# Optimization experiments

Hardware: AMD Instinct MI355X
Metric: run time of the kernel (lower is better)

Reference implementation:

```python
import jax, jax.numpy as jnp
import numpy as np

N, L, S, H, E, D = 4, 1024, 1024, 16, 64, 64
NUM_POS = 2  # adjacency matrix: 0 = not adjacent, 1 = adjacent


def setup_inputs() -> dict:
    key = jax.random.key(0)
    kq, kk, kv, kt, kp = jax.random.split(key, 5)
    return {
        "queries": jax.random.normal(kq, (N, L, H, E), dtype=jnp.float32),
        "keys": jax.random.normal(kk, (N, S, H, E), dtype=jnp.float32),
        "values": jax.random.normal(kv, (N, S, H, D), dtype=jnp.float32),
        "attn_mask": jnp.zeros((L, S), dtype=jnp.float32),          # additive attention mask
        "key_len_mask": jnp.zeros((N, S), dtype=jnp.float32),       # additive key-length mask
        "pos_table": jax.random.normal(kt, (NUM_POS, H), dtype=jnp.float32),  # per-head graph pos bias
        "pos": jax.random.randint(kp, (N, L, S), 0, NUM_POS),        # adjacency matrix
    }


def reference(queries, keys, values, attn_mask, key_len_mask, pos_table, pos):
    E_dim = queries.shape[-1]
    softmax_temp = 1.0 / jnp.sqrt(jnp.asarray(E_dim, dtype=queries.dtype))
    # scores: [N, H, L, S]
    QK = jnp.einsum("nlhe,nshe->nhls", queries, keys)
    QK = QK + attn_mask[None, None, :, :]
    QK = QK + key_len_mask[:, None, None, :]
    QK = softmax_temp * QK
    # graph positional encoding: per-head bias looked up from adjacency matrix
    # pos_table[pos] -> [N, L, S, H] -> [N, H, L, S]
    QK = QK + jnp.transpose(pos_table[pos], (0, 3, 1, 2))
    A = jax.nn.softmax(QK, axis=-1)  # dropout is identity in eval/reference
    V = jnp.einsum("nhls,nshd->nlhd", A, values)
    return V
```

## Files before the change

kernel.cpp:

```cpp
#include <hip/hip_runtime.h>


typedef __attribute__((ext_vector_type(8))) __bf16 bf16x8;
typedef __attribute__((ext_vector_type(16))) float f32x16;
typedef __attribute__((ext_vector_type(4))) unsigned int u32x4;

#define TEMP2 (0.125f * 1.4426950408889634f)
#define LG2E 1.4426950408889634f

static __device__ __forceinline__ unsigned short f2bf(float x) {
  unsigned int u = __builtin_bit_cast(unsigned int, x);
  u += 0x7FFFu + ((u >> 16) & 1u);
  return (unsigned short)(u >> 16);
}
static __device__ __forceinline__ unsigned int cvtpk(float lo, float hi) {
  unsigned int r;
  asm("v_cvt_pk_bf16_f32 %0, %1, %2" : "=v"(r) : "v"(lo), "v"(hi));
  return r;
}
static __device__ __forceinline__ void gload16(const void* g, void* l) {
  __builtin_amdgcn_global_load_lds((const __attribute__((address_space(1))) void*)g,
                                   (__attribute__((address_space(3))) void*)l, 16, 0, 0);
}
static __device__ __forceinline__ void plswap(unsigned int& a, unsigned int& b) {
  asm("v_permlane32_swap_b32 %0, %1" : "+v"(a), "+v"(b));
}

__global__ __launch_bounds__(256) void k_prep(
    const int* __restrict__ pos, unsigned int* __restrict__ pospk,
    const float* __restrict__ K, unsigned short* __restrict__ Kp,
    const float* __restrict__ V, unsigned short* __restrict__ Vt,
    const float* __restrict__ mask, const float* __restrict__ klm,
    int* __restrict__ cmflag) {
  __shared__ float ld[64][65];
  int b = blockIdx.x;
  int tid = threadIdx.x;
  if (b < 256) {
    int idx = b * 256 + tid;
    int s = (idx >> 4) & 1023;
    const float* src = K + idx * 64;
    unsigned short row[64];
#pragma unroll
    for (int j = 0; j < 16; ++j) {
      float4 v = *(const float4*)(src + j * 4);
      row[j*4+0] = f2bf(v.x); row[j*4+1] = f2bf(v.y);
      row[j*4+2] = f2bf(v.z); row[j*4+3] = f2bf(v.w);
    }
    int n = idx >> 14, h = idx & 15;
    unsigned short* dst = Kp + ((n * 16 + h) * 1024 + s) * 64;
#pragma unroll
    for (int bb = 0; bb < 8; ++bb) {
      int pb = bb ^ (s & 7);
      *(u32x4*)(dst + pb * 8) = *(const u32x4*)(&row[bb * 8]);
    }
  } else if (b < 1280) {
    int vb = b - 256;
    int t = vb & 15, h = (vb >> 4) & 15, n = vb >> 8;
    {
      int s = tid >> 2, dq = (tid & 3) * 16;
      const float* src = V + ((n * 1024 + t * 64 + s) * 16 + h) * 64 + dq;
#pragma unroll
      for (int j = 0; j < 4; ++j) {
        float4 v = *(const float4*)(src + j * 4);
        ld[s][dq + j*4 + 0] = v.x; ld[s][dq + j*4 + 1] = v.y;
        ld[s][dq + j*4 + 2] = v.z; ld[s][dq + j*4 + 3] = v.w;
      }
    }
    __syncthreads();
    {
      int d = tid >> 2, sq = (tid & 3) * 16;
      unsigned short vals[16];
#pragma unroll
      for (int k = 0; k < 16; ++k) vals[k] = f2bf(ld[sq + k][d]);
      unsigned short* dst = Vt + ((n * 16 + h) * 64 + d) * 1024 + t * 64;
#pragma unroll
      for (int cb = 0; cb < 2; ++cb) {
        int blk = (sq >> 3) + cb;
        int pb = blk ^ (d & 7);
        *(u32x4*)(dst + pb * 8) = *(const u32x4*)(&vals[cb * 8]);
      }
    }
  } else if (b < 1536) {
    if (!cmflag) return;
    int base = ((b - 1280) * 256 + tid) * 16;
    const float* m = mask + base;
    float acc = 0.f;
#pragma unroll
    for (int j = 0; j < 4; ++j) {
      float4 v = *(const float4*)(m + j * 4);
      acc += __builtin_fabsf(v.x) + __builtin_fabsf(v.y) +
             __builtin_fabsf(v.z) + __builtin_fabsf(v.w);
    }
    unsigned long long bal = __ballot(acc != 0.f);
    if ((tid & 63) == 0 && bal != 0ull) atomicOr(cmflag, 1);
  } else if (b == 1536) {
    if (!cmflag) return;
    const float* m = klm + tid * 16;
    float acc = 0.f;
#pragma unroll
    for (int j = 0; j < 4; ++j) {
      float4 v = *(const float4*)(m + j * 4);
      acc += __builtin_fabsf(v.x) + __builtin_fabsf(v.y) +
             __builtin_fabsf(v.z) + __builtin_fabsf(v.w);
    }
    unsigned long long bal = __ballot(acc != 0.f);
    if ((tid & 63) == 0 && bal != 0ull) atomicOr(cmflag, 1);
  } else {
    int gi = (b - 1537) * 256 + tid;
    int v = pos[gi];
    unsigned long long m = __ballot(v & 1);
    int lane = tid & 63;
    if (lane == 0 || lane == 32) {
      int n = gi >> 20, l = (gi >> 10) & 1023, sw = (gi & 1023) >> 5;
      pospk[(n * 32 + sw) * 1024 + l] =
          (lane == 0) ? (unsigned int)m : (unsigned int)(m >> 32);
    }
  }
}

__global__ __launch_bounds__(512) void k_attn(
    const float* __restrict__ Q, const float* __restrict__ mask,
    const float* __restrict__ klm, const float* __restrict__ ptab,
    const unsigned int* __restrict__ pospk,
    const unsigned short* __restrict__ Kp, const unsigned short* __restrict__ Vt,
    const int* __restrict__ cmf,
    float* __restrict__ out) {
  __shared__ __align__(16) unsigned short KBA[2][4096];
  __shared__ __align__(16) unsigned short KBB[2][4096];
  __shared__ __align__(16) unsigned short VBA[2][4096];
  __shared__ __align__(16) unsigned short VBB[2][4096];
  __shared__ __align__(16) unsigned short VBC[2][4096];

  int bid = blockIdx.x;
  int nh = bid & 63;
  int n = nh >> 4, h = nh & 15, lblk = bid >> 6;
  int tid = threadIdx.x;
  int w8 = tid >> 6, lane = tid & 63;
  int g = w8 >> 2, w4 = w8 & 3;
  int l31 = lane & 31, h5 = lane >> 5;
  int l = lblk * 128 + w4 * 32 + l31;
  const int hcm = cmf ? *cmf : 1;

  const float* qrow = Q + ((n * 1024 + l) * 16 + h) * 64;
  bf16x8 qf[4];
#pragma unroll
  for (int ke = 0; ke < 4; ++ke) {
    float4 a = *(const float4*)(qrow + ke * 16 + h5 * 8);
    float4 bq = *(const float4*)(qrow + ke * 16 + h5 * 8 + 4);
    u32x4 pk;
    pk[0] = cvtpk(a.x * TEMP2, a.y * TEMP2);
    pk[1] = cvtpk(a.z * TEMP2, a.w * TEMP2);
    pk[2] = cvtpk(bq.x * TEMP2, bq.y * TEMP2);
    pk[3] = cvtpk(bq.z * TEMP2, bq.w * TEMP2);
    qf[ke] = __builtin_bit_cast(bf16x8, pk);
  }
  const float delta2 = (ptab[16 + h] - ptab[h]) * LG2E;

  float mrun = -1e30f, lrun = 0.f;
  f32x16 Oc0 = {0,0,0,0,0,0,0,0,0,0,0,0,0,0,0,0};
  f32x16 Oc1 = {0,0,0,0,0,0,0,0,0,0,0,0,0,0,0,0};
  u32x4 pfA = {0,0,0,0}, pfB = {0,0,0,0}, pfC = {0,0,0,0}, pfD = {0,0,0,0};

  const unsigned short* KpB = Kp + nh * 65536;
  const unsigned short* VtB = Vt + nh * 65536;
  const float* mrowB = mask + l * 1024 + g * 512;
  const float* krowB = klm + n * 1024 + g * 512;
  const unsigned int* posB = pospk + (n * 32 + g * 16) * 1024 + l;
  const int h4 = h5 * 4;

  const int x7 = l31 & 7;
  const int co0 = ((0 + h5) ^ x7) * 8;
  const int co1 = ((2 + h5) ^ x7) * 8;
  const int co2 = ((4 + h5) ^ x7) * 8;
  const int co3 = ((6 + h5) ^ x7) * 8;
  const int rb = l31 * 64;

  const unsigned short* kS = KpB + g * 32768 + w4 * 1024 + lane * 8;
  const unsigned short* vS = VtB + (w4 * 16 + (lane >> 3)) * 1024 + g * 512 + (lane & 7) * 8;
  const int kD = w4 * 1024 + lane * 8;

#define BF(x) __builtin_bit_cast(bf16x8, x)
#define MFMA(A, B, C) __builtin_amdgcn_mfma_f32_32x32x16_bf16(A, B, C, 0, 0, 0)
#define LDB(ARR, OFF) BF(*(const u32x4*)&ARR[g][(OFF)])

#pragma unroll
  for (int j = 0; j < 2; ++j) {
    gload16(kS + j * 512, &KBA[g][kD + j * 512]);
    gload16(vS + j * 8192, &VBA[g][kD + j * 512]);
  }
  __syncthreads();

#define BODY(T, KR, KW, VR, VW, DO_PV, STG)                                    \
  {                                                                            \
    unsigned pwx = posB[((T) * 2) * 1024];                  \
    unsigned pwy = posB[((T) * 2 + 1) * 1024];                                 \
          \
    if (STG) {                                                                 \
      _Pragma("unroll")                                                        \
      for (int j = 0; j < 2; ++j) {                                            \
        gload16(kS + ((T) + 1) * 4096 + j * 512, &KW[g][kD + j * 512]);        \
        gload16(vS + ((T) + 1) * 64 + j * 8192, &VW[g][kD + j * 512]);         \
      }                                                                        \
    }                                                                          \
                     \
    f32x16 sv0 = {0,0,0,0,0,0,0,0,0,0,0,0,0,0,0,0};                            \
    f32x16 sv1 = {0,0,0,0,0,0,0,0,0,0,0,0,0,0,0,0};                            \
    __builtin_amdgcn_s_setprio(1);                                             \
    sv0 = MFMA(LDB(KR, rb + co0), qf[0], sv0);                                 \
    sv1 = MFMA(LDB(KR, rb + 2048 + co0), qf[0], sv1);                          \
    if (DO_PV) {                                                               \
      Oc0 = MFMA(LDB(VR, rb + co0), BF(pfA), Oc0);                             \
      Oc1 = MFMA(LDB(VR, rb + 2048 + co0), BF(pfA), Oc1);                      \
    }                                                                          \
    sv0 = MFMA(LDB(KR, rb + co1), qf[1], sv0);                                 \
    sv1 = MFMA(LDB(KR, rb + 2048 + co1), qf[1], sv1);                          \
    if (DO_PV) {                                                               \
      Oc0 = MFMA(LDB(VR, rb + co1), BF(pfB), Oc0);                             \
      Oc1 = MFMA(LDB(VR, rb + 2048 + co1), BF(pfB), Oc1);                      \
    }                                                                          \
    sv0 = MFMA(LDB(KR, rb + co2), qf[2], sv0);                                 \
    sv1 = MFMA(LDB(KR, rb + 2048 + co2), qf[2], sv1);                          \
    if (DO_PV) {                                                               \
      Oc0 = MFMA(LDB(VR, rb + co2), BF(pfC), Oc0);                             \
      Oc1 = MFMA(LDB(VR, rb + 2048 + co2), BF(pfC), Oc1);                      \
    }                                                                          \
    sv0 = MFMA(LDB(KR, rb + co3), qf[3], sv0);                                 \
    sv1 = MFMA(LDB(KR, rb + 2048 + co3), qf[3], sv1);                          \
    if (DO_PV) {                                                               \
      Oc0 = MFMA(LDB(VR, rb + co3), BF(pfD), Oc0);                             \
      Oc1 = MFMA(LDB(VR, rb + 2048 + co3), BF(pfD), Oc1);                      \
    }                                                                          \
    __builtin_amdgcn_s_setprio(0);                                             \
               \
    if (hcm) {                                                                 \
      _Pragma("unroll")                                                        \
      for (int r2 = 0; r2 < 4; ++r2) {                                         \
        float4 mv0 = *(const float4*)(mrowB + (T) * 64 + r2 * 8 + h4);         \
        float4 kv0 = *(const float4*)(krowB + (T) * 64 + r2 * 8 + h4);         \
        float4 mv1 = *(const float4*)(mrowB + (T) * 64 + 32 + r2 * 8 + h4);    \
        float4 kv1 = *(const float4*)(krowB + (T) * 64 + 32 + r2 * 8 + h4);    \
        sv0[r2 * 4 + 0] += (mv0.x + kv0.x) * TEMP2;                            \
        sv0[r2 * 4 + 1] += (mv0.y + kv0.y) * TEMP2;                            \
        sv0[r2 * 4 + 2] += (mv0.z + kv0.z) * TEMP2;                            \
        sv0[r2 * 4 + 3] += (mv0.w + kv0.w) * TEMP2;                            \
        sv1[r2 * 4 + 0] += (mv1.x + kv1.x) * TEMP2;                            \
        sv1[r2 * 4 + 1] += (mv1.y + kv1.y) * TEMP2;                            \
        sv1[r2 * 4 + 2] += (mv1.z + kv1.z) * TEMP2;                            \
        sv1[r2 * 4 + 3] += (mv1.w + kv1.w) * TEMP2;                            \
      }                                                                        \
    }                                                                          \
    {                                                                          \
      unsigned pws0 = pwx >> h4;                                               \
      unsigned pws1 = pwy >> h4;                                               \
      _Pragma("unroll")                                                        \
      for (int r2 = 0; r2 < 4; ++r2)                                           \
        _Pragma("unroll")                                                      \
        for (int i = 0; i < 4; ++i) {                                          \
          float bit0 = (float)((pws0 >> (r2 * 8 + i)) & 1u);                   \
          float bit1 = (float)((pws1 >> (r2 * 8 + i)) & 1u);                   \
          sv0[r2 * 4 + i] = fmaf(bit0, delta2, sv0[r2 * 4 + i]);               \
          sv1[r2 * 4 + i] = fmaf(bit1, delta2, sv1[r2 * 4 + i]);               \
        }                                                                      \
    }                                                                          \
                      \
    {                                                                          \
      float m8[8];                                                             \
      _Pragma("unroll")                                                        \
      for (int i = 0; i < 8; ++i)                                              \
        m8[i] = fmaxf(fmaxf(sv0[2 * i], sv0[2 * i + 1]),                       \
                      fmaxf(sv1[2 * i], sv1[2 * i + 1]));                      \
      float m4a = fmaxf(m8[0], m8[1]), m4b = fmaxf(m8[2], m8[3]);              \
      float m4c = fmaxf(m8[4], m8[5]), m4d = fmaxf(m8[6], m8[7]);              \
      float tmax = fmaxf(fmaxf(m4a, m4b), fmaxf(m4c, m4d));                    \
      tmax = fmaxf(tmax, __shfl_xor(tmax, 32));                                \
      if (!__all(tmax <= mrun + 4.0f)) {                                       \
        float mnew = fmaxf(mrun, tmax);                                        \
        float sc = __builtin_amdgcn_exp2f(mrun - mnew);                        \
        lrun *= sc;                                                            \
        Oc0 *= sc; Oc1 *= sc;                                                  \
        mrun = mnew;                                                           \
      }                                                                        \
      float s8[8];                                                             \
      _Pragma("unroll")                                                        \
      for (int i = 0; i < 8; ++i) {                                            \
        float p0 = __builtin_amdgcn_exp2f(sv0[2 * i] - mrun);                  \
        float p1 = __builtin_amdgcn_exp2f(sv0[2 * i + 1] - mrun);              \
        float p2 = __builtin_amdgcn_exp2f(sv1[2 * i] - mrun);                  \
        float p3 = __builtin_amdgcn_exp2f(sv1[2 * i + 1] - mrun);              \
        sv0[2 * i] = p0; sv0[2 * i + 1] = p1;                                  \
        sv1[2 * i] = p2; sv1[2 * i + 1] = p3;                                  \
        s8[i] = (p0 + p1) + (p2 + p3);                                         \
      }                                                                        \
      float s4a = s8[0] + s8[1], s4b = s8[2] + s8[3];                          \
      float s4c = s8[4] + s8[5], s4d = s8[6] + s8[7];                          \
      lrun += (s4a + s4b) + (s4c + s4d);    \
    }                                                                          \
                    \
    {                                                                          \
      unsigned a0 = cvtpk(sv0[0], sv0[1]),   a1 = cvtpk(sv0[2], sv0[3]);       \
      unsigned a2 = cvtpk(sv0[4], sv0[5]),   a3 = cvtpk(sv0[6], sv0[7]);       \
      plswap(a0, a2); plswap(a1, a3);                                          \
      pfA[0] = a0; pfA[1] = a1; pfA[2] = a2; pfA[3] = a3;                      \
      unsigned b0_ = cvtpk(sv0[8], sv0[9]),   b1_ = cvtpk(sv0[10], sv0[11]);   \
      unsigned b2_ = cvtpk(sv0[12], sv0[13]), b3_ = cvtpk(sv0[14], sv0[15]);   \
      plswap(b0_, b2_); plswap(b1_, b3_);                                      \
      pfB[0] = b0_; pfB[1] = b1_; pfB[2] = b2_; pfB[3] = b3_;                  \
      unsigned c0 = cvtpk(sv1[0], sv1[1]),   c1 = cvtpk(sv1[2], sv1[3]);       \
      unsigned c2 = cvtpk(sv1[4], sv1[5]),   c3 = cvtpk(sv1[6], sv1[7]);       \
      plswap(c0, c2); plswap(c1, c3);                                          \
      pfC[0] = c0; pfC[1] = c1; pfC[2] = c2; pfC[3] = c3;                      \
      unsigned d0 = cvtpk(sv1[8], sv1[9]),   d1 = cvtpk(sv1[10], sv1[11]);     \
      unsigned d2 = cvtpk(sv1[12], sv1[13]), d3 = cvtpk(sv1[14], sv1[15]);     \
      plswap(d0, d2); plswap(d1, d3);                                          \
      pfD[0] = d0; pfD[1] = d1; pfD[2] = d2; pfD[3] = d3;                      \
    }                                                                          \
    if (STG) __syncthreads();        \
  }

  BODY( 0, KBA, KBB, VBA, VBB, 0, 1)
  BODY( 1, KBB, KBA, VBA, VBC, 1, 1)
  BODY( 2, KBA, KBB, VBB, VBA, 1, 1)
  BODY( 3, KBB, KBA, VBC, VBB, 1, 1)
  BODY( 4, KBA, KBB, VBA, VBC, 1, 1)
  BODY( 5, KBB, KBA, VBB, VBA, 1, 1)
  BODY( 6, KBA, KBB, VBC, VBB, 1, 1)
  BODY( 7, KBB, KBB, VBA, VBB, 1, 0)
#undef BODY

  __builtin_amdgcn_s_setprio(1);
  Oc0 = MFMA(LDB(VBB, rb + co0), BF(pfA), Oc0);
  Oc1 = MFMA(LDB(VBB, rb + 2048 + co0), BF(pfA), Oc1);
  Oc0 = MFMA(LDB(VBB, rb + co1), BF(pfB), Oc0);
  Oc1 = MFMA(LDB(VBB, rb + 2048 + co1), BF(pfB), Oc1);
  Oc0 = MFMA(LDB(VBB, rb + co2), BF(pfC), Oc0);
  Oc1 = MFMA(LDB(VBB, rb + 2048 + co2), BF(pfC), Oc1);
  Oc0 = MFMA(LDB(VBB, rb + co3), BF(pfD), Oc0);
  Oc1 = MFMA(LDB(VBB, rb + 2048 + co3), BF(pfD), Oc1);
  __builtin_amdgcn_s_setprio(0);
#undef MFMA
#undef BF
#undef LDB

  float lw = lrun + __shfl_xor(lrun, 32);
  __syncthreads();
#pragma unroll
  for (int r = 0; r < 2; ++r) {
    if (g == 1 && (w4 >> 1) == r) {
      float* row = ((w4 & 1) ? (float*)VBB : (float*)VBA) + lane * 36;
#pragma unroll
      for (int r2 = 0; r2 < 4; ++r2) {
        *(float4*)(row + r2 * 4) =
            make_float4(Oc0[4*r2+0], Oc0[4*r2+1], Oc0[4*r2+2], Oc0[4*r2+3]);
        *(float4*)(row + 16 + r2 * 4) =
            make_float4(Oc1[4*r2+0], Oc1[4*r2+1], Oc1[4*r2+2], Oc1[4*r2+3]);
      }
      row[32] = mrun;
      row[33] = lw;
    }
    __syncthreads();
    if (g == 0 && (w4 >> 1) == r) {
      const float* row = ((w4 & 1) ? (float*)VBB : (float*)VBA) + lane * 36;
      float m1 = row[32], l1 = row[33];
      float mm = fmaxf(mrun, m1);
      float s0e = __builtin_amdgcn_exp2f(mrun - mm);
      float s1e = __builtin_amdgcn_exp2f(m1 - mm);
      float ltot = lw * s0e + l1 * s1e;
      float inv = 1.0f / ltot;
      float* orow = out + ((n * 1024 + l) * 16 + h) * 64;
#pragma unroll
      for (int r2 = 0; r2 < 4; ++r2) {
        float4 o;
        o.x = (Oc0[4*r2+0] * s0e + row[r2*4+0] * s1e) * inv;
        o.y = (Oc0[4*r2+1] * s0e + row[r2*4+1] * s1e) * inv;
        o.z = (Oc0[4*r2+2] * s0e + row[r2*4+2] * s1e) * inv;
        o.w = (Oc0[4*r2+3] * s0e + row[r2*4+3] * s1e) * inv;
        *(float4*)(orow + r2 * 8 + h4) = o;
        o.x = (Oc1[4*r2+0] * s0e + row[16+r2*4+0] * s1e) * inv;
        o.y = (Oc1[4*r2+1] * s0e + row[16+r2*4+1] * s1e) * inv;
        o.z = (Oc1[4*r2+2] * s0e + row[16+r2*4+2] * s1e) * inv;
        o.w = (Oc1[4*r2+3] * s0e + row[16+r2*4+3] * s1e) * inv;
        *(float4*)(orow + 32 + r2 * 8 + h4) = o;
      }
    }
    __syncthreads();
  }
}

extern "C" void kernel_launch(void* const* d_in, const int* in_sizes, int n_in,
                              void* d_out, int out_size, void* d_ws, size_t ws_size,
                              hipStream_t stream) {
  const float* Q    = (const float*)d_in[0];
  const float* K    = (const float*)d_in[1];
  const float* V    = (const float*)d_in[2];
  const float* mask = (const float*)d_in[3];
  const float* klm  = (const float*)d_in[4];
  const float* ptab = (const float*)d_in[5];
  const int*   pos  = (const int*)d_in[6];
  float* out = (float*)d_out;

  char* ws = (char*)d_ws;
  unsigned int*   pospk = (unsigned int*)ws;
  unsigned short* Kp    = (unsigned short*)(ws + (1 << 19));
  unsigned short* Vt    = (unsigned short*)(ws + (1 << 19) + (8 << 20));
  int*            cmf   = (int*)(ws + (1 << 19) + (16 << 20));
  const size_t need_flag = (size_t)(1 << 19) + (size_t)(16 << 20) + 64;
  const bool use_flag = ws_size >= need_flag;
  if (!use_flag) cmf = nullptr;

  if (use_flag) hipMemsetAsync(cmf, 0, 4, stream);
  k_prep<<<17921, 256, 0, stream>>>(pos, pospk, K, Kp, V, Vt, mask, klm, cmf);
  k_attn<<<512, 512, 0, stream>>>(Q, mask, klm, ptab, pospk, Kp, Vt, cmf, out);
}
```

Baseline: 64.38 us.

## Fuse prep and attention into one cooperative kernel with grid sync

Replaces the memset, the prep kernel and the attention kernel with a single cooperative launch. In the first phase each block converts K to bf16, transposes V through LDS, packs adjacency bits and checks whether any mask is nonzero. A grid-wide sync then lets the same blocks run the attention body, which is turned into a shared macro. The aim is to remove two extra launches and the inter-kernel gap. The cost is a grid barrier, and the fused kernel needs at least two resident blocks per CU; if that check or the cooperative launch fails, it falls back to the old path.

```diff
diff --git a/kernel.cpp b/kernel.cpp
--- a/kernel.cpp
+++ b/kernel.cpp
@@ -1,5 +1,8 @@
 #include <hip/hip_runtime.h>
-
+#include <hip/hip_cooperative_groups.h>
+
+
+namespace cg = cooperative_groups;
 
 typedef __attribute__((ext_vector_type(8))) __bf16 bf16x8;
 typedef __attribute__((ext_vector_type(16))) float f32x16;
@@ -118,83 +121,124 @@
   }
 }
 
-__global__ __launch_bounds__(512) void k_attn(
-    const float* __restrict__ Q, const float* __restrict__ mask,
-    const float* __restrict__ klm, const float* __restrict__ ptab,
-    const unsigned int* __restrict__ pospk,
-    const unsigned short* __restrict__ Kp, const unsigned short* __restrict__ Vt,
-    const int* __restrict__ cmf,
-    float* __restrict__ out) {
-  __shared__ __align__(16) unsigned short KBA[2][4096];
-  __shared__ __align__(16) unsigned short KBB[2][4096];
-  __shared__ __align__(16) unsigned short VBA[2][4096];
-  __shared__ __align__(16) unsigned short VBB[2][4096];
-  __shared__ __align__(16) unsigned short VBC[2][4096];
-
-  int bid = blockIdx.x;
-  int nh = bid & 63;
-  int n = nh >> 4, h = nh & 15, lblk = bid >> 6;
-  int tid = threadIdx.x;
-  int w8 = tid >> 6, lane = tid & 63;
-  int g = w8 >> 2, w4 = w8 & 3;
-  int l31 = lane & 31, h5 = lane >> 5;
-  int l = lblk * 128 + w4 * 32 + l31;
-  const int hcm = cmf ? *cmf : 1;
-
-  const float* qrow = Q + ((n * 1024 + l) * 16 + h) * 64;
-  bf16x8 qf[4];
-#pragma unroll
-  for (int ke = 0; ke < 4; ++ke) {
-    float4 a = *(const float4*)(qrow + ke * 16 + h5 * 8);
-    float4 bq = *(const float4*)(qrow + ke * 16 + h5 * 8 + 4);
-    u32x4 pk;
-    pk[0] = cvtpk(a.x * TEMP2, a.y * TEMP2);
-    pk[1] = cvtpk(a.z * TEMP2, a.w * TEMP2);
-    pk[2] = cvtpk(bq.x * TEMP2, bq.y * TEMP2);
-    pk[3] = cvtpk(bq.z * TEMP2, bq.w * TEMP2);
-    qf[ke] = __builtin_bit_cast(bf16x8, pk);
-  }
-  const float delta2 = (ptab[16 + h] - ptab[h]) * LG2E;
-
-  float mrun = -1e30f, lrun = 0.f;
-  f32x16 Oc0 = {0,0,0,0,0,0,0,0,0,0,0,0,0,0,0,0};
-  f32x16 Oc1 = {0,0,0,0,0,0,0,0,0,0,0,0,0,0,0,0};
-  u32x4 pfA = {0,0,0,0}, pfB = {0,0,0,0}, pfC = {0,0,0,0}, pfD = {0,0,0,0};
-
-  const unsigned short* KpB = Kp + nh * 65536;
-  const unsigned short* VtB = Vt + nh * 65536;
-  const float* mrowB = mask + l * 1024 + g * 512;
-  const float* krowB = klm + n * 1024 + g * 512;
-  const unsigned int* posB = pospk + (n * 32 + g * 16) * 1024 + l;
-  const int h4 = h5 * 4;
-
-  const int x7 = l31 & 7;
-  const int co0 = ((0 + h5) ^ x7) * 8;
-  const int co1 = ((2 + h5) ^ x7) * 8;
-  const int co2 = ((4 + h5) ^ x7) * 8;
-  const int co3 = ((6 + h5) ^ x7) * 8;
-  const int rb = l31 * 64;
-
-  const unsigned short* kS = KpB + g * 32768 + w4 * 1024 + lane * 8;
-  const unsigned short* vS = VtB + (w4 * 16 + (lane >> 3)) * 1024 + g * 512 + (lane & 7) * 8;
-  const int kD = w4 * 1024 + lane * 8;
+#define ATTN_MAIN(HCMEXPR)                                                     \
+  int nh = bid & 63;                                                           \
+  int n = nh >> 4, h = nh & 15, lblk = bid >> 6;                               \
+  int w8 = tid >> 6, lane = tid & 63;                                          \
+  int g = w8 >> 2, w4 = w8 & 3;                                                \
+  int l31 = lane & 31, h5 = lane >> 5;                                         \
+  int l = lblk * 128 + w4 * 32 + l31;                                          \
+  const int hcm = (HCMEXPR);                                                   \
+  const float* qrow = Q + ((n * 1024 + l) * 16 + h) * 64;                      \
+  bf16x8 qf[4];                                                                \
+  _Pragma("unroll")                                                            \
+  for (int ke = 0; ke < 4; ++ke) {                                             \
+    float4 a = *(const float4*)(qrow + ke * 16 + h5 * 8);                      \
+    float4 bq = *(const float4*)(qrow + ke * 16 + h5 * 8 + 4);                 \
+    u32x4 pk;                                                                  \
+    pk[0] = cvtpk(a.x * TEMP2, a.y * TEMP2);                                   \
+    pk[1] = cvtpk(a.z * TEMP2, a.w * TEMP2);                                   \
+    pk[2] = cvtpk(bq.x * TEMP2, bq.y * TEMP2);                                 \
+    pk[3] = cvtpk(bq.z * TEMP2, bq.w * TEMP2);                                 \
+    qf[ke] = __builtin_bit_cast(bf16x8, pk);                                   \
+  }                                                                            \
+  const float delta2 = (ptab[16 + h] - ptab[h]) * LG2E;                        \
+  float mrun = -1e30f, lrun = 0.f;                                             \
+  f32x16 Oc0 = {0,0,0,0,0,0,0,0,0,0,0,0,0,0,0,0};                              \
+  f32x16 Oc1 = {0,0,0,0,0,0,0,0,0,0,0,0,0,0,0,0};                              \
+  u32x4 pfA = {0,0,0,0}, pfB = {0,0,0,0}, pfC = {0,0,0,0}, pfD = {0,0,0,0};    \
+  const unsigned short* KpB = Kp + nh * 65536;                                 \
+  const unsigned short* VtB = Vt + nh * 65536;                                 \
+  const float* mrowB = mask + l * 1024 + g * 512;                              \
+  const float* krowB = klm + n * 1024 + g * 512;                               \
+  const unsigned int* posB = pospk + (n * 32 + g * 16) * 1024 + l;             \
+  const int h4 = h5 * 4;                                                       \
+  const int x7 = l31 & 7;                                                      \
+  const int co0 = ((0 + h5) ^ x7) * 8;                                         \
+  const int co1 = ((2 + h5) ^ x7) * 8;                                         \
+  const int co2 = ((4 + h5) ^ x7) * 8;                                         \
+  const int co3 = ((6 + h5) ^ x7) * 8;                                         \
+  const int rb = l31 * 64;                                                     \
+  const unsigned short* kS = KpB + g * 32768 + w4 * 1024 + lane * 8;           \
+  const unsigned short* vS = VtB + (w4 * 16 + (lane >> 3)) * 1024 + g * 512 +  \
+                             (lane & 7) * 8;                                   \
+  const int kD = w4 * 1024 + lane * 8;                                         \
+  _Pragma("unroll")                                                            \
+  for (int j = 0; j < 2; ++j) {                                                \
+    gload16(kS + j * 512, &KBA[g][kD + j * 512]);                              \
+    gload16(vS + j * 8192, &VBA[g][kD + j * 512]);                             \
+  }                                                                            \
+  __syncthreads();                                                             \
+  BODY( 0, KBA, KBB, VBA, VBB, 0, 1)                                           \
+  BODY( 1, KBB, KBA, VBA, VBC, 1, 1)                                           \
+  BODY( 2, KBA, KBB, VBB, VBA, 1, 1)                                           \
+  BODY( 3, KBB, KBA, VBC, VBB, 1, 1)                                           \
+  BODY( 4, KBA, KBB, VBA, VBC, 1, 1)                                           \
+  BODY( 5, KBB, KBA, VBB, VBA, 1, 1)                                           \
+  BODY( 6, KBA, KBB, VBC, VBB, 1, 1)                                           \
+  BODY( 7, KBB, KBB, VBA, VBB, 1, 0)                                           \
+  __builtin_amdgcn_s_setprio(1);                                               \
+  Oc0 = MFMA(LDB(VBB, rb + co0), BF(pfA), Oc0);                                \
+  Oc1 = MFMA(LDB(VBB, rb + 2048 + co0), BF(pfA), Oc1);                         \
+  Oc0 = MFMA(LDB(VBB, rb + co1), BF(pfB), Oc0);                                \
+  Oc1 = MFMA(LDB(VBB, rb + 2048 + co1), BF(pfB), Oc1);                         \
+  Oc0 = MFMA(LDB(VBB, rb + co2), BF(pfC), Oc0);                                \
+  Oc1 = MFMA(LDB(VBB, rb + 2048 + co2), BF(pfC), Oc1);                         \
+  Oc0 = MFMA(LDB(VBB, rb + co3), BF(pfD), Oc0);                                \
+  Oc1 = MFMA(LDB(VBB, rb + 2048 + co3), BF(pfD), Oc1);                         \
+  __builtin_amdgcn_s_setprio(0);                                               \
+  float lw = lrun + __shfl_xor(lrun, 32);                                      \
+  __syncthreads();                                                             \
+  _Pragma("unroll")                                                            \
+  for (int r = 0; r < 2; ++r) {                                                \
+    if (g == 1 && (w4 >> 1) == r) {                                            \
+      float* row = ((w4 & 1) ? (float*)VBB : (float*)VBA) + lane * 36;         \
+      _Pragma("unroll")                                                        \
+      for (int r2 = 0; r2 < 4; ++r2) {                                         \
+        *(float4*)(row + r2 * 4) =                                             \
+            make_float4(Oc0[4*r2+0], Oc0[4*r2+1], Oc0[4*r2+2], Oc0[4*r2+3]);   \
+        *(float4*)(row + 16 + r2 * 4) =                                        \
+            make_float4(Oc1[4*r2+0], Oc1[4*r2+1], Oc1[4*r2+2], Oc1[4*r2+3]);   \
+      }                                                                        \
+      row[32] = mrun;                                                          \
+      row[33] = lw;                                                            \
+    }                                                                          \
+    __syncthreads();                                                           \
+    if (g == 0 && (w4 >> 1) == r) {                                            \
+      const float* row = ((w4 & 1) ? (float*)VBB : (float*)VBA) + lane * 36;   \
+      float m1 = row[32], l1 = row[33];                                        \
+      float mm = fmaxf(mrun, m1);                                              \
+      float s0e = __builtin_amdgcn_exp2f(mrun - mm);                           \
+      float s1e = __builtin_amdgcn_exp2f(m1 - mm);                             \
+      float ltot = lw * s0e + l1 * s1e;                                        \
+      float inv = 1.0f / ltot;                                                 \
+      float* orow = out + ((n * 1024 + l) * 16 + h) * 64;                      \
+      _Pragma("unroll")                                                        \
+      for (int r2 = 0; r2 < 4; ++r2) {                                         \
+        float4 o;                                                              \
+        o.x = (Oc0[4*r2+0] * s0e + row[r2*4+0] * s1e) * inv;                   \
+        o.y = (Oc0[4*r2+1] * s0e + row[r2*4+1] * s1e) * inv;                   \
+        o.z = (Oc0[4*r2+2] * s0e + row[r2*4+2] * s1e) * inv;                   \
+        o.w = (Oc0[4*r2+3] * s0e + row[r2*4+3] * s1e) * inv;                   \
+        *(float4*)(orow + r2 * 8 + h4) = o;                                    \
+        o.x = (Oc1[4*r2+0] * s0e + row[16+r2*4+0] * s1e) * inv;                \
+        o.y = (Oc1[4*r2+1] * s0e + row[16+r2*4+1] * s1e) * inv;                \
+        o.z = (Oc1[4*r2+2] * s0e + row[16+r2*4+2] * s1e) * inv;                \
+        o.w = (Oc1[4*r2+3] * s0e + row[16+r2*4+3] * s1e) * inv;                \
+        *(float4*)(orow + 32 + r2 * 8 + h4) = o;                               \
+      }                                                                        \
+    }                                                                          \
+    __syncthreads();                                                           \
+  }
 
 #define BF(x) __builtin_bit_cast(bf16x8, x)
 #define MFMA(A, B, C) __builtin_amdgcn_mfma_f32_32x32x16_bf16(A, B, C, 0, 0, 0)
 #define LDB(ARR, OFF) BF(*(const u32x4*)&ARR[g][(OFF)])
 
-#pragma unroll
-  for (int j = 0; j < 2; ++j) {
-    gload16(kS + j * 512, &KBA[g][kD + j * 512]);
-    gload16(vS + j * 8192, &VBA[g][kD + j * 512]);
-  }
-  __syncthreads();
-
 #define BODY(T, KR, KW, VR, VW, DO_PV, STG)                                    \
   {                                                                            \
-    unsigned pwx = posB[((T) * 2) * 1024];                  \
+    unsigned pwx = posB[((T) * 2) * 1024];                                     \
     unsigned pwy = posB[((T) * 2 + 1) * 1024];                                 \
-          \
     if (STG) {                                                                 \
       _Pragma("unroll")                                                        \
       for (int j = 0; j < 2; ++j) {                                            \
@@ -202,7 +246,6 @@
         gload16(vS + ((T) + 1) * 64 + j * 8192, &VW[g][kD + j * 512]);         \
       }                                                                        \
     }                                                                          \
-                     \
     f32x16 sv0 = {0,0,0,0,0,0,0,0,0,0,0,0,0,0,0,0};                            \
     f32x16 sv1 = {0,0,0,0,0,0,0,0,0,0,0,0,0,0,0,0};                            \
     __builtin_amdgcn_s_setprio(1);                                             \
@@ -231,7 +274,6 @@
       Oc1 = MFMA(LDB(VR, rb + 2048 + co3), BF(pfD), Oc1);                      \
     }                                                                          \
     __builtin_amdgcn_s_setprio(0);                                             \
-               \
     if (hcm) {                                                                 \
       _Pragma("unroll")                                                        \
       for (int r2 = 0; r2 < 4; ++r2) {                                         \
@@ -262,7 +304,6 @@
           sv1[r2 * 4 + i] = fmaf(bit1, delta2, sv1[r2 * 4 + i]);               \
         }                                                                      \
     }                                                                          \
-                      \
     {                                                                          \
       float m8[8];                                                             \
       _Pragma("unroll")                                                        \
@@ -293,9 +334,8 @@
       }                                                                        \
       float s4a = s8[0] + s8[1], s4b = s8[2] + s8[3];                          \
       float s4c = s8[4] + s8[5], s4d = s8[6] + s8[7];                          \
-      lrun += (s4a + s4b) + (s4c + s4d);    \
-    }                                                                          \
-                    \
+      lrun += (s4a + s4b) + (s4c + s4d);                                       \
+    }                                                                          \
     {                                                                          \
       unsigned a0 = cvtpk(sv0[0], sv0[1]),   a1 = cvtpk(sv0[2], sv0[3]);       \
       unsigned a2 = cvtpk(sv0[4], sv0[5]),   a3 = cvtpk(sv0[6], sv0[7]);       \
@@ -314,76 +354,149 @@
       plswap(d0, d2); plswap(d1, d3);                                          \
       pfD[0] = d0; pfD[1] = d1; pfD[2] = d2; pfD[3] = d3;                      \
     }                                                                          \
-    if (STG) __syncthreads();        \
-  }
-
-  BODY( 0, KBA, KBB, VBA, VBB, 0, 1)
-  BODY( 1, KBB, KBA, VBA, VBC, 1, 1)
-  BODY( 2, KBA, KBB, VBB, VBA, 1, 1)
-  BODY( 3, KBB, KBA, VBC, VBB, 1, 1)
-  BODY( 4, KBA, KBB, VBA, VBC, 1, 1)
-  BODY( 5, KBB, KBA, VBB, VBA, 1, 1)
-  BODY( 6, KBA, KBB, VBC, VBB, 1, 1)
-  BODY( 7, KBB, KBB, VBA, VBB, 1, 0)
-#undef BODY
-
-  __builtin_amdgcn_s_setprio(1);
-  Oc0 = MFMA(LDB(VBB, rb + co0), BF(pfA), Oc0);
-  Oc1 = MFMA(LDB(VBB, rb + 2048 + co0), BF(pfA), Oc1);
-  Oc0 = MFMA(LDB(VBB, rb + co1), BF(pfB), Oc0);
-  Oc1 = MFMA(LDB(VBB, rb + 2048 + co1), BF(pfB), Oc1);
-  Oc0 = MFMA(LDB(VBB, rb + co2), BF(pfC), Oc0);
-  Oc1 = MFMA(LDB(VBB, rb + 2048 + co2), BF(pfC), Oc1);
-  Oc0 = MFMA(LDB(VBB, rb + co3), BF(pfD), Oc0);
-  Oc1 = MFMA(LDB(VBB, rb + 2048 + co3), BF(pfD), Oc1);
-  __builtin_amdgcn_s_setprio(0);
-#undef MFMA
-#undef BF
-#undef LDB
-
-  float lw = lrun + __shfl_xor(lrun, 32);
-  __syncthreads();
-#pragma unroll
-  for (int r = 0; r < 2; ++r) {
-    if (g == 1 && (w4 >> 1) == r) {
-      float* row = ((w4 & 1) ? (float*)VBB : (float*)VBA) + lane * 36;
-#pragma unroll
-      for (int r2 = 0; r2 < 4; ++r2) {
-        *(float4*)(row + r2 * 4) =
-            make_float4(Oc0[4*r2+0], Oc0[4*r2+1], Oc0[4*r2+2], Oc0[4*r2+3]);
-        *(float4*)(row + 16 + r2 * 4) =
-            make_float4(Oc1[4*r2+0], Oc1[4*r2+1], Oc1[4*r2+2], Oc1[4*r2+3]);
+    if (STG) __syncthreads();                                                  \
+  }
+
+__global__ __launch_bounds__(512) void k_attn(
+    const float* __restrict__ Q, const float* __restrict__ mask,
+    const float* __restrict__ klm, const float* __restrict__ ptab,
+    const unsigned int* __restrict__ pospk,
+    const unsigned short* __restrict__ Kp, const unsigned short* __restrict__ Vt,
+    const int* __restrict__ cmf,
+    float* __restrict__ out) {
+  __shared__ __align__(16) unsigned short KBA[2][4096];
+  __shared__ __align__(16) unsigned short KBB[2][4096];
+  __shared__ __align__(16) unsigned short VBA[2][4096];
+  __shared__ __align__(16) unsigned short VBB[2][4096];
+  __shared__ __align__(16) unsigned short VBC[2][4096];
+  int bid = blockIdx.x;
+  int tid = threadIdx.x;
+  ATTN_MAIN(cmf ? *cmf : 1)
+}
+
+__global__ __launch_bounds__(512) void k_fused(
+    const float* __restrict__ Q, const float* __restrict__ K,
+    const float* __restrict__ V, const float* __restrict__ mask,
+    const float* __restrict__ klm, const float* __restrict__ ptab,
+    const int* __restrict__ pos,
+    unsigned int* __restrict__ pospk, unsigned short* __restrict__ Kp,
+    unsigned short* __restrict__ Vt, int* __restrict__ flags,
+    float* __restrict__ out) {
+  __shared__ __align__(16) unsigned short KBA[2][4096];
+  __shared__ __align__(16) unsigned short KBB[2][4096];
+  __shared__ __align__(16) unsigned short VBA[2][4096];
+  __shared__ __align__(16) unsigned short VBB[2][4096];
+  __shared__ __align__(16) unsigned short VBC[2][4096];
+
+  int bid = blockIdx.x;
+  int tid = threadIdx.x;
+  int gt = bid * 512 + tid;
+
+  {
+    int row = gt >> 2, q = gt & 3;
+    int s = (row >> 4) & 1023;
+    const float* src = K + row * 64 + q * 16;
+    unsigned short rv[16];
+#pragma unroll
+    for (int j = 0; j < 4; ++j) {
+      float4 v = *(const float4*)(src + j * 4);
+      rv[j*4+0] = f2bf(v.x); rv[j*4+1] = f2bf(v.y);
+      rv[j*4+2] = f2bf(v.z); rv[j*4+3] = f2bf(v.w);
+    }
+    int n = row >> 14, h = row & 15;
+    unsigned short* dst = Kp + ((n * 16 + h) * 1024 + s) * 64;
+#pragma unroll
+    for (int c = 0; c < 2; ++c) {
+      int bb = q * 2 + c;
+      int pb = bb ^ (s & 7);
+      *(u32x4*)(dst + pb * 8) = *(const u32x4*)(&rv[c * 8]);
+    }
+  }
+  float acc = 0.f;
+  {
+    const float* m = mask + gt * 4;
+    float4 v = *(const float4*)m;
+    acc += __builtin_fabsf(v.x) + __builtin_fabsf(v.y) +
+           __builtin_fabsf(v.z) + __builtin_fabsf(v.w);
+    if (gt < 1024) {
+      float4 kv = *(const float4*)(klm + gt * 4);
+      acc += __builtin_fabsf(kv.x) + __builtin_fabsf(kv.y) +
+             __builtin_fabsf(kv.z) + __builtin_fabsf(kv.w);
+    }
+  }
+  {
+    int r = bid * 8 + (tid >> 6);
+    int n = r >> 10, l = r & 1023;
+    int lane = tid & 63;
+    const int* prow = pos + r * 1024 + lane;
+#pragma unroll
+    for (int j = 0; j < 16; ++j) {
+      unsigned long long m = __ballot(prow[j * 64] & 1);
+      if (lane == 0) pospk[(n * 32 + 2 * j) * 1024 + l] = (unsigned int)m;
+      else if (lane == 32) pospk[(n * 32 + 2 * j + 1) * 1024 + l] = (unsigned int)(m >> 32);
+    }
+  }
+  {
+    float* ld = (float*)KBA;
+#pragma unroll
+    for (int tt = 0; tt < 2; ++tt) {
+      int vt = bid * 2 + tt;
+      int t16 = vt & 15, h = (vt >> 4) & 15, n = vt >> 8;
+#pragma unroll
+      for (int hf = 0; hf < 2; ++hf) {
+        __syncthreads();
+        {
+          int sl = (tid >> 4), dq = (tid & 15) * 4;
+          int s_glob = t16 * 64 + hf * 32 + sl;
+          float4 v = *(const float4*)(V + ((n * 1024 + s_glob) * 16 + h) * 64 + dq);
+          ld[sl * 65 + dq + 0] = v.x; ld[sl * 65 + dq + 1] = v.y;
+          ld[sl * 65 + dq + 2] = v.z; ld[sl * 65 + dq + 3] = v.w;
+        }
+        __syncthreads();
+        if (tid < 256) {
+          int d = tid >> 2, bq = (tid & 3) + hf * 4;
+          int sl0 = (tid & 3) * 8;
+          unsigned short vals[8];
+#pragma unroll
+          for (int k = 0; k < 8; ++k) vals[k] = f2bf(ld[(sl0 + k) * 65 + d]);
+          int pb = bq ^ (d & 7);
+          unsigned short* dst = Vt + ((n * 16 + h) * 64 + d) * 1024 + t16 * 64;
+          *(u32x4*)(dst + pb * 8) = *(const u32x4*)(&vals[0]);
+        }
       }
-      row[32] = mrun;
-      row[33] = lw;
-    }
+    }
+  }
+  {
     __syncthreads();
-    if (g == 0 && (w4 >> 1) == r) {
-      const float* row = ((w4 & 1) ? (float*)VBB : (float*)VBA) + lane * 36;
-      float m1 = row[32], l1 = row[33];
-      float mm = fmaxf(mrun, m1);
-      float s0e = __builtin_amdgcn_exp2f(mrun - mm);
-      float s1e = __builtin_amdgcn_exp2f(m1 - mm);
-      float ltot = lw * s0e + l1 * s1e;
-      float inv = 1.0f / ltot;
-      float* orow = out + ((n * 1024 + l) * 16 + h) * 64;
-#pragma unroll
-      for (int r2 = 0; r2 < 4; ++r2) {
-        float4 o;
-        o.x = (Oc0[4*r2+0] * s0e + row[r2*4+0] * s1e) * inv;
-        o.y = (Oc0[4*r2+1] * s0e + row[r2*4+1] * s1e) * inv;
-        o.z = (Oc0[4*r2+2] * s0e + row[r2*4+2] * s1e) * inv;
-        o.w = (Oc0[4*r2+3] * s0e + row[r2*4+3] * s1e) * inv;
-        *(float4*)(orow + r2 * 8 + h4) = o;
-        o.x = (Oc1[4*r2+0] * s0e + row[16+r2*4+0] * s1e) * inv;
-        o.y = (Oc1[4*r2+1] * s0e + row[16+r2*4+1] * s1e) * inv;
-        o.z = (Oc1[4*r2+2] * s0e + row[16+r2*4+2] * s1e) * inv;
-        o.w = (Oc1[4*r2+3] * s0e + row[16+r2*4+3] * s1e) * inv;
-        *(float4*)(orow + 32 + r2 * 8 + h4) = o;
-      }
-    }
+    unsigned long long bal = __ballot(acc != 0.f);
+    int* wf = (int*)KBB;
+    if ((tid & 63) == 0) wf[tid >> 6] = (bal != 0ull) ? 1 : 0;
     __syncthreads();
-  }
+    if (tid == 0) {
+      int v = 0;
+#pragma unroll
+      for (int i = 0; i < 8; ++i) v |= wf[i];
+      flags[bid] = v;
+    }
+  }
+  __threadfence();
+  cg::this_grid().sync();
+
+  int hcmg;
+  {
+    int v = flags[tid];
+    unsigned long long bal = __ballot(v != 0);
+    int* wf = (int*)KBB;
+    if ((tid & 63) == 0) wf[tid >> 6] = (bal != 0ull) ? 1 : 0;
+    __syncthreads();
+    int r = 0;
+#pragma unroll
+    for (int i = 0; i < 8; ++i) r |= wf[i];
+    hcmg = r;
+    __syncthreads();
+  }
+
+  ATTN_MAIN(hcmg)
 }
 
 extern "C" void kernel_launch(void* const* d_in, const int* in_sizes, int n_in,
@@ -402,12 +515,32 @@
   unsigned int*   pospk = (unsigned int*)ws;
   unsigned short* Kp    = (unsigned short*)(ws + (1 << 19));
   unsigned short* Vt    = (unsigned short*)(ws + (1 << 19) + (8 << 20));
-  int*            cmf   = (int*)(ws + (1 << 19) + (16 << 20));
-  const size_t need_flag = (size_t)(1 << 19) + (size_t)(16 << 20) + 64;
-  const bool use_flag = ws_size >= need_flag;
-  if (!use_flag) cmf = nullptr;
-
-  if (use_flag) hipMemsetAsync(cmf, 0, 4, stream);
-  k_prep<<<17921, 256, 0, stream>>>(pos, pospk, K, Kp, V, Vt, mask, klm, cmf);
-  k_attn<<<512, 512, 0, stream>>>(Q, mask, klm, ptab, pospk, Kp, Vt, cmf, out);
-}
+  int*            flags = (int*)(ws + (1 << 19) + (16 << 20));
+  const size_t need = (size_t)(1 << 19) + (size_t)(16 << 20) + 2048;
+  const bool ws_ok = ws_size >= need;
+
+  bool coop_done = false;
+  if (ws_ok) {
+    int maxb = 0;
+    hipError_t qe = hipOccupancyMaxActiveBlocksPerMultiprocessor(
+        &maxb, (const void*)k_fused, 512, 0);
+    if (qe == hipSuccess && maxb >= 2) {
+      void* args[] = {(void*)&Q, (void*)&K, (void*)&V, (void*)&mask,
+                      (void*)&klm, (void*)&ptab, (void*)&pos, (void*)&pospk,
+                      (void*)&Kp, (void*)&Vt, (void*)&flags, (void*)&out};
+      hipError_t le = hipLaunchCooperativeKernel((const void*)k_fused,
+                                                 dim3(512), dim3(512), args,
+                                                 0, stream);
+      if (le == hipSuccess) coop_done = true;
+      else (void)hipGetLastError();
+    } else {
+      (void)hipGetLastError();
+    }
+  }
+  if (!coop_done) {
+    int* cmf = ws_ok ? flags : nullptr;
+    if (ws_ok) hipMemsetAsync(cmf, 0, 4, stream);
+    k_prep<<<17921, 256, 0, stream>>>(pos, pospk, K, Kp, V, Vt, mask, klm, cmf);
+    k_attn<<<512, 512, 0, stream>>>(Q, mask, klm, ptab, pospk, Kp, Vt, cmf, out);
+  }
+}
```

Measured after the change: 64.37 us. No clear change (-0.0%).

## Merge prep work into uniform 512-block kernel, replace atomic flag with per-block flags

Applied to the files above, without the earlier changes.

The heterogeneous 17921-block prep kernel is replaced by a 512-block kernel in which every block does a slice of K conversion, mask scanning, pos bit-packing and V transposition. The memset plus global atomicOr mask flag is replaced by per-block flags that the attention kernel reduces with a block-wide ballot at startup. This removes a memset launch and many tiny blocks, at the cost of a longer per-block prep body with extra syncthreads and a small flag reduction at the start of every attention block.

```diff
diff --git a/kernel.cpp b/kernel.cpp
--- a/kernel.cpp
+++ b/kernel.cpp
@@ -26,94 +26,97 @@
   asm("v_permlane32_swap_b32 %0, %1" : "+v"(a), "+v"(b));
 }
 
-__global__ __launch_bounds__(256) void k_prep(
+__global__ __launch_bounds__(512) void k_prep2(
     const int* __restrict__ pos, unsigned int* __restrict__ pospk,
     const float* __restrict__ K, unsigned short* __restrict__ Kp,
     const float* __restrict__ V, unsigned short* __restrict__ Vt,
     const float* __restrict__ mask, const float* __restrict__ klm,
-    int* __restrict__ cmflag) {
-  __shared__ float ld[64][65];
-  int b = blockIdx.x;
-  int tid = threadIdx.x;
-  if (b < 256) {
-    int idx = b * 256 + tid;
-    int s = (idx >> 4) & 1023;
-    const float* src = K + idx * 64;
-    unsigned short row[64];
+    int* __restrict__ flags) {
+  __shared__ float ld[32][65];
+  __shared__ int wf[8];
+  int bid = blockIdx.x, tid = threadIdx.x;
+  int gt = bid * 512 + tid;
+
+  {
+    int row = gt >> 2, q = gt & 3;
+    int s = (row >> 4) & 1023;
+    const float* src = K + row * 64 + q * 16;
+    unsigned short rv[16];
+#pragma unroll
+    for (int j = 0; j < 4; ++j) {
+      float4 v = *(const float4*)(src + j * 4);
+      rv[j*4+0] = f2bf(v.x); rv[j*4+1] = f2bf(v.y);
+      rv[j*4+2] = f2bf(v.z); rv[j*4+3] = f2bf(v.w);
+    }
+    int n = row >> 14, h = row & 15;
+    unsigned short* dst = Kp + ((n * 16 + h) * 1024 + s) * 64;
+#pragma unroll
+    for (int c = 0; c < 2; ++c) {
+      int bb = q * 2 + c;
+      int pb = bb ^ (s & 7);
+      *(u32x4*)(dst + pb * 8) = *(const u32x4*)(&rv[c * 8]);
+    }
+  }
+  float acc = 0.f;
+  {
+    float4 v = *(const float4*)(mask + gt * 4);
+    acc += __builtin_fabsf(v.x) + __builtin_fabsf(v.y) +
+           __builtin_fabsf(v.z) + __builtin_fabsf(v.w);
+    if (gt < 1024) {
+      float4 kv = *(const float4*)(klm + gt * 4);
+      acc += __builtin_fabsf(kv.x) + __builtin_fabsf(kv.y) +
+             __builtin_fabsf(kv.z) + __builtin_fabsf(kv.w);
+    }
+  }
+  {
+    int r = bid * 8 + (tid >> 6);
+    int n = r >> 10, l = r & 1023;
+    int lane = tid & 63;
+    const int* prow = pos + r * 1024 + lane;
 #pragma unroll
     for (int j = 0; j < 16; ++j) {
-      float4 v = *(const float4*)(src + j * 4);
-      row[j*4+0] = f2bf(v.x); row[j*4+1] = f2bf(v.y);
-      row[j*4+2] = f2bf(v.z); row[j*4+3] = f2bf(v.w);
-    }
-    int n = idx >> 14, h = idx & 15;
-    unsigned short* dst = Kp + ((n * 16 + h) * 1024 + s) * 64;
-#pragma unroll
-    for (int bb = 0; bb < 8; ++bb) {
-      int pb = bb ^ (s & 7);
-      *(u32x4*)(dst + pb * 8) = *(const u32x4*)(&row[bb * 8]);
-    }
-  } else if (b < 1280) {
-    int vb = b - 256;
-    int t = vb & 15, h = (vb >> 4) & 15, n = vb >> 8;
-    {
-      int s = tid >> 2, dq = (tid & 3) * 16;
-      const float* src = V + ((n * 1024 + t * 64 + s) * 16 + h) * 64 + dq;
-#pragma unroll
-      for (int j = 0; j < 4; ++j) {
-        float4 v = *(const float4*)(src + j * 4);
-        ld[s][dq + j*4 + 0] = v.x; ld[s][dq + j*4 + 1] = v.y;
-        ld[s][dq + j*4 + 2] = v.z; ld[s][dq + j*4 + 3] = v.w;
+      unsigned long long m = __ballot(prow[j * 64] & 1);
+      if (lane == 0) pospk[(n * 32 + 2 * j) * 1024 + l] = (unsigned int)m;
+      else if (lane == 32) pospk[(n * 32 + 2 * j + 1) * 1024 + l] = (unsigned int)(m >> 32);
+    }
+  }
+#pragma unroll
+  for (int tt = 0; tt < 2; ++tt) {
+    int vt = bid * 2 + tt;
+    int t16 = vt & 15, h = (vt >> 4) & 15, n = vt >> 8;
+#pragma unroll
+    for (int hf = 0; hf < 2; ++hf) {
+      __syncthreads();
+      {
+        int sl = tid >> 4, dq = (tid & 15) * 4;
+        int s_glob = t16 * 64 + hf * 32 + sl;
+        float4 v = *(const float4*)(V + ((n * 1024 + s_glob) * 16 + h) * 64 + dq);
+        ld[sl][dq + 0] = v.x; ld[sl][dq + 1] = v.y;
+        ld[sl][dq + 2] = v.z; ld[sl][dq + 3] = v.w;
       }
-    }
+      __syncthreads();
+      if (tid < 256) {
+        int d = tid >> 2, bq = (tid & 3) + hf * 4;
+        int sl0 = (tid & 3) * 8;
+        unsigned short vals[8];
+#pragma unroll
+        for (int k = 0; k < 8; ++k) vals[k] = f2bf(ld[sl0 + k][d]);
+        int pb = bq ^ (d & 7);
+        unsigned short* dst = Vt + ((n * 16 + h) * 64 + d) * 1024 + t16 * 64;
+        *(u32x4*)(dst + pb * 8) = *(const u32x4*)(&vals[0]);
+      }
+    }
+  }
+  __syncthreads();
+  {
+    unsigned long long bal = __ballot(acc != 0.f);
+    if ((tid & 63) == 0) wf[tid >> 6] = (bal != 0ull) ? 1 : 0;
     __syncthreads();
-    {
-      int d = tid >> 2, sq = (tid & 3) * 16;
-      unsigned short vals[16];
-#pragma unroll
-      for (int k = 0; k < 16; ++k) vals[k] = f2bf(ld[sq + k][d]);
-      unsigned short* dst = Vt + ((n * 16 + h) * 64 + d) * 1024 + t * 64;
-#pragma unroll
-      for (int cb = 0; cb < 2; ++cb) {
-        int blk = (sq >> 3) + cb;
-        int pb = blk ^ (d & 7);
-        *(u32x4*)(dst + pb * 8) = *(const u32x4*)(&vals[cb * 8]);
-      }
-    }
-  } else if (b < 1536) {
-    if (!cmflag) return;
-    int base = ((b - 1280) * 256 + tid) * 16;
-    const float* m = mask + base;
-    float acc = 0.f;
-#pragma unroll
-    for (int j = 0; j < 4; ++j) {
-      float4 v = *(const float4*)(m + j * 4);
-      acc += __builtin_fabsf(v.x) + __builtin_fabsf(v.y) +
-             __builtin_fabsf(v.z) + __builtin_fabsf(v.w);
-    }
-    unsigned long long bal = __ballot(acc != 0.f);
-    if ((tid & 63) == 0 && bal != 0ull) atomicOr(cmflag, 1);
-  } else if (b == 1536) {
-    if (!cmflag) return;
-    const float* m = klm + tid * 16;
-    float acc = 0.f;
-#pragma unroll
-    for (int j = 0; j < 4; ++j) {
-      float4 v = *(const float4*)(m + j * 4);
-      acc += __builtin_fabsf(v.x) + __builtin_fabsf(v.y) +
-             __builtin_fabsf(v.z) + __builtin_fabsf(v.w);
-    }
-    unsigned long long bal = __ballot(acc != 0.f);
-    if ((tid & 63) == 0 && bal != 0ull) atomicOr(cmflag, 1);
-  } else {
-    int gi = (b - 1537) * 256 + tid;
-    int v = pos[gi];
-    unsigned long long m = __ballot(v & 1);
-    int lane = tid & 63;
-    if (lane == 0 || lane == 32) {
-      int n = gi >> 20, l = (gi >> 10) & 1023, sw = (gi & 1023) >> 5;
-      pospk[(n * 32 + sw) * 1024 + l] =
-          (lane == 0) ? (unsigned int)m : (unsigned int)(m >> 32);
+    if (tid == 0 && flags) {
+      int v = 0;
+#pragma unroll
+      for (int i = 0; i < 8; ++i) v |= wf[i];
+      flags[bid] = v;
     }
   }
 }
@@ -123,7 +126,7 @@
     const float* __restrict__ klm, const float* __restrict__ ptab,
     const unsigned int* __restrict__ pospk,
     const unsigned short* __restrict__ Kp, const unsigned short* __restrict__ Vt,
-    const int* __restrict__ cmf,
+    const int* __restrict__ flags,
     float* __restrict__ out) {
   __shared__ __align__(16) unsigned short KBA[2][4096];
   __shared__ __align__(16) unsigned short KBB[2][4096];
@@ -132,14 +135,29 @@
   __shared__ __align__(16) unsigned short VBC[2][4096];
 
   int bid = blockIdx.x;
+  int tid = threadIdx.x;
+
+  int hcmg = 1;
+  if (flags) {
+    int v = flags[tid];
+    unsigned long long bal = __ballot(v != 0);
+    int* wf = (int*)KBB;
+    if ((tid & 63) == 0) wf[tid >> 6] = (bal != 0ull) ? 1 : 0;
+    __syncthreads();
+    int r = 0;
+#pragma unroll
+    for (int i = 0; i < 8; ++i) r |= wf[i];
+    hcmg = r;
+    __syncthreads();
+  }
+
   int nh = bid & 63;
   int n = nh >> 4, h = nh & 15, lblk = bid >> 6;
-  int tid = threadIdx.x;
   int w8 = tid >> 6, lane = tid & 63;
   int g = w8 >> 2, w4 = w8 & 3;
   int l31 = lane & 31, h5 = lane >> 5;
   int l = lblk * 128 + w4 * 32 + l31;
-  const int hcm = cmf ? *cmf : 1;
+  const int hcm = hcmg;
 
   const float* qrow = Q + ((n * 1024 + l) * 16 + h) * 64;
   bf16x8 qf[4];
@@ -192,9 +210,8 @@
 
 #define BODY(T, KR, KW, VR, VW, DO_PV, STG)                                    \
   {                                                                            \
-    unsigned pwx = posB[((T) * 2) * 1024];                  \
+    unsigned pwx = posB[((T) * 2) * 1024];                                     \
     unsigned pwy = posB[((T) * 2 + 1) * 1024];                                 \
-          \
     if (STG) {                                                                 \
       _Pragma("unroll")                                                        \
       for (int j = 0; j < 2; ++j) {                                            \
@@ -202,7 +219,6 @@
         gload16(vS + ((T) + 1) * 64 + j * 8192, &VW[g][kD + j * 512]);         \
       }                                                                        \
     }                                                                          \
-                     \
     f32x16 sv0 = {0,0,0,0,0,0,0,0,0,0,0,0,0,0,0,0};                            \
     f32x16 sv1 = {0,0,0,0,0,0,0,0,0,0,0,0,0,0,0,0};                            \
     __builtin_amdgcn_s_setprio(1);                                             \
@@ -231,7 +247,6 @@
       Oc1 = MFMA(LDB(VR, rb + 2048 + co3), BF(pfD), Oc1);                      \
     }                                                                          \
     __builtin_amdgcn_s_setprio(0);                                             \
-               \
     if (hcm) {                                                                 \
       _Pragma("unroll")                                                        \
       for (int r2 = 0; r2 < 4; ++r2) {                                         \
@@ -262,7 +277,6 @@
           sv1[r2 * 4 + i] = fmaf(bit1, delta2, sv1[r2 * 4 + i]);               \
         }                                                                      \
     }                                                                          \
-                      \
     {                                                                          \
       float m8[8];                                                             \
       _Pragma("unroll")                                                        \
@@ -293,9 +307,8 @@
       }                                                                        \
       float s4a = s8[0] + s8[1], s4b = s8[2] + s8[3];                          \
       float s4c = s8[4] + s8[5], s4d = s8[6] + s8[7];                          \
-      lrun += (s4a + s4b) + (s4c + s4d);    \
-    }                                                                          \
-                    \
+      lrun += (s4a + s4b) + (s4c + s4d);                                       \
+    }                                                                          \
     {                                                                          \
       unsigned a0 = cvtpk(sv0[0], sv0[1]),   a1 = cvtpk(sv0[2], sv0[3]);       \
       unsigned a2 = cvtpk(sv0[4], sv0[5]),   a3 = cvtpk(sv0[6], sv0[7]);       \
@@ -314,7 +327,7 @@
       plswap(d0, d2); plswap(d1, d3);                                          \
       pfD[0] = d0; pfD[1] = d1; pfD[2] = d2; pfD[3] = d3;                      \
     }                                                                          \
-    if (STG) __syncthreads();        \
+    if (STG) __syncthreads();                                                  \
   }
 
   BODY( 0, KBA, KBB, VBA, VBB, 0, 1)
@@ -402,12 +415,10 @@
   unsigned int*   pospk = (unsigned int*)ws;
   unsigned short* Kp    = (unsigned short*)(ws + (1 << 19));
   unsigned short* Vt    = (unsigned short*)(ws + (1 << 19) + (8 << 20));
-  int*            cmf   = (int*)(ws + (1 << 19) + (16 << 20));
-  const size_t need_flag = (size_t)(1 << 19) + (size_t)(16 << 20) + 64;
-  const bool use_flag = ws_size >= need_flag;
-  if (!use_flag) cmf = nullptr;
-
-  if (use_flag) hipMemsetAsync(cmf, 0, 4, stream);
-  k_prep<<<17921, 256, 0, stream>>>(pos, pospk, K, Kp, V, Vt, mask, klm, cmf);
-  k_attn<<<512, 512, 0, stream>>>(Q, mask, klm, ptab, pospk, Kp, Vt, cmf, out);
-}
+  int*            flags = (int*)(ws + (1 << 19) + (16 << 20));
+  const size_t need = (size_t)(1 << 19) + (size_t)(16 << 20) + 2048;
+  if (ws_size < need) flags = nullptr;
+
+  k_prep2<<<512, 512, 0, stream>>>(pos, pospk, K, Kp, V, Vt, mask, klm, flags);
+  k_attn<<<512, 512, 0, stream>>>(Q, mask, klm, ptab, pospk, Kp, Vt, flags, out);
+}
```

New measurement: 55.64 us, median of 2. 1.16x faster.
